# Kernel tuning notes

Hardware: AMD Instinct MI355X
Metric: run time of the kernel (lower is better)

The kernel has to match this reference:

```python
import jax, jax.numpy as jnp
import numpy as np

D = 256      # d_model
NH = 8       # num_heads
NP = 4       # n_points
H = 100      # feature map height (single level)
W = 100      # feature map width
B = 4
Q = H * W
S = H * W


def setup_inputs() -> dict:
    key = jax.random.key(0)
    ks = jax.random.split(key, 12)
    p = lambda k, shp, s=0.02: jax.random.normal(k, shp, jnp.float32) * s
    return {
        "hidden_states": jax.random.normal(ks[0], (B, Q, D), jnp.float32),
        "encoder_hidden_states": jax.random.normal(ks[1], (B, S, D), jnp.float32),
        "reference_points": jax.random.uniform(ks[2], (B, Q, 1, 2), jnp.float32),
        "spatial_shapes": jnp.array([[H, W]], dtype=jnp.int32),
        "W_off": p(ks[3], (NH * NP * 2, D)),
        "b_off": p(ks[4], (NH * NP * 2,), 0.5),
        "W_attn": p(ks[5], (NH * NP, D)),
        "b_attn": jnp.zeros((NH * NP,), jnp.float32),
        "W_val": p(ks[6], (D, D)),
        "b_val": jnp.zeros((D,), jnp.float32),
        "W_out": p(ks[7], (D, D)),
        "b_out": jnp.zeros((D,), jnp.float32),
    }


def _deform_attn(hidden_states, encoder_hidden_states, reference_points,
                 W_off, b_off, W_attn, b_attn, W_val, b_val, W_out, b_out):
    Bsz, Qn, Dm = hidden_states.shape
    d = Dm // NH

    # value projection -> [B, NH, S, d]
    value = (encoder_hidden_states @ W_val.T + b_val).reshape(Bsz, S, NH, d)
    vflat = value.transpose(0, 2, 1, 3).reshape(Bsz * NH, H * W, d)

    # sampling offsets [B,Q,NH,NP,2] (n_levels=1 squeezed)
    off = (hidden_states @ W_off.T + b_off).reshape(Bsz, Qn, NH, NP, 2)
    # attention weights softmax over (n_levels*n_points)=NP -> [B,Q,NH,NP]
    attn = jax.nn.softmax((hidden_states @ W_attn.T + b_attn).reshape(Bsz, Qn, NH, NP), axis=-1)

    # normalized sampling locations: ref + off / [W, H]
    normalizer = jnp.array([W, H], jnp.float32)
    # reference_points: [B,Q,1,2] (level dim) -> broadcast over heads/points
    loc = reference_points[:, :, None, 0, None, :] + off / normalizer  # [B,Q,NH,NP,2]

    # grid_sample semantics: grid = 2*loc - 1, align_corners=False, zeros padding
    gx = 2.0 * loc[..., 0] - 1.0
    gy = 2.0 * loc[..., 1] - 1.0
    x = ((gx + 1.0) * W - 1.0) * 0.5   # pixel coords [B,Q,NH,NP]
    y = ((gy + 1.0) * H - 1.0) * 0.5
    x0 = jnp.floor(x); y0 = jnp.floor(y)
    x1 = x0 + 1.0;     y1 = y0 + 1.0
    wx1 = x - x0; wx0 = 1.0 - wx1
    wy1 = y - y0; wy0 = 1.0 - wy1

    bh = jnp.arange(Bsz * NH)[:, None]

    def corner(xi, yi, wgt):
        valid = (xi >= 0) & (xi <= W - 1) & (yi >= 0) & (yi <= H - 1)
        xi_c = jnp.clip(xi, 0, W - 1).astype(jnp.int32)
        yi_c = jnp.clip(yi, 0, H - 1).astype(jnp.int32)
        idx = (yi_c * W + xi_c).transpose(0, 2, 1, 3).reshape(Bsz * NH, Qn * NP)
        g = vflat[bh, idx]  # [B*NH, Q*NP, d]
        wv = (wgt * valid.astype(wgt.dtype)).transpose(0, 2, 1, 3).reshape(Bsz * NH, Qn * NP, 1)
        return g * wv

    sampled = corner(x0, y0, wx0 * wy0)
    sampled = sampled + corner(x1, y0, wx1 * wy0)
    sampled = sampled + corner(x0, y1, wx0 * wy1)
    sampled = sampled + corner(x1, y1, wx1 * wy1)
    sampled = sampled.reshape(Bsz, NH, Qn, NP, d)

    out = jnp.einsum("bhqpd,bqhp->bqhd", sampled, attn).reshape(Bsz, Qn, Dm)
    return out @ W_out.T + b_out


def reference(hidden_states, encoder_hidden_states, reference_points, spatial_shapes,
              W_off, b_off, W_attn, b_attn, W_val, b_val, W_out, b_out):
    # spatial_shapes is static metadata (must equal [[H, W]]); shapes are baked in.
    return _deform_attn(hidden_states, encoder_hidden_states, reference_points,
                        W_off, b_off, W_attn, b_attn, W_val, b_val, W_out, b_out)
```

## Files before the change

### kernel.cpp

```cpp
#include <hip/hip_runtime.h>

constexpr int HH = 100;
constexpr int WW = 100;
constexpr int NH = 8;
constexpr int NP = 4;
constexpr int B  = 4;
constexpr int Q  = HH * WW;
constexpr int S  = Q;
constexpr int K  = 256;
constexpr int DH = 32;
constexpr int M  = B * Q;
constexpr int NTILES = M / 32;

typedef __attribute__((ext_vector_type(8))) short short8;
typedef __attribute__((ext_vector_type(4))) float f32x4;

__device__ inline unsigned short f2bf(float f) {
    unsigned u = __builtin_bit_cast(unsigned, f);
    u += 0x7fffu + ((u >> 16) & 1u);
    return (unsigned short)(u >> 16);
}
__device__ inline float bf2f(unsigned short h) {
    return __builtin_bit_cast(float, ((unsigned)h) << 16);
}
__device__ inline unsigned short f2h(float f) {
    _Float16 h = (_Float16)f;
    return __builtin_bit_cast(unsigned short, h);
}
__device__ inline float h2f(unsigned short u) {
    return (float)__builtin_bit_cast(_Float16, u);
}

__device__ inline void lds_st16s(short* base, int row, int stride, int kcol, short8 v) {
    *reinterpret_cast<short8*>(&base[row * stride + (kcol ^ ((row & 7) << 3))]) = v;
}
__device__ inline short8 lds_ld16s(const short* base, int row, int stride, int kcol) {
    return *reinterpret_cast<const short8*>(&base[row * stride + (kcol ^ ((row & 7) << 3))]);
}

__device__ inline short8 cvt8(float4 a, float4 b) {
    short8 r;
    r[0] = (short)f2bf(a.x); r[1] = (short)f2bf(a.y);
    r[2] = (short)f2bf(a.z); r[3] = (short)f2bf(a.w);
    r[4] = (short)f2bf(b.x); r[5] = (short)f2bf(b.y);
    r[6] = (short)f2bf(b.z); r[7] = (short)f2bf(b.w);
    return r;
}

__global__ __launch_bounds__(1024) void stage1(
    const float* __restrict__ enc, const float* __restrict__ Wval,
    const float* __restrict__ bval, unsigned short* __restrict__ vflat,
    const float* __restrict__ hidden, const float* __restrict__ Woff,
    const float* __restrict__ Wattn, const float* __restrict__ boff,
    const float* __restrict__ battn, unsigned short* __restrict__ proj)
{
    __shared__ __align__(16) short SM[73728];
    short* Bs = SM;
    short* As = SM + 65536;

    const int tid  = threadIdx.x;
    const int lane = tid & 63, w = tid >> 6;
    const int l15  = lane & 15, l4 = lane >> 4;
    const int arow = tid >> 5, ak = (tid & 31) * 8;

    constexpr int NV = 143, NJ = 113;

    if (blockIdx.x < NV) {
        int t = blockIdx.x;
        float4 fa0, fa1;
        auto lda = [&](int tt) {
            const float* s = &enc[(size_t)(tt * 32 + arow) * K + ak];
            fa0 = *reinterpret_cast<const float4*>(s);
            fa1 = *reinterpret_cast<const float4*>(s + 4);
        };
        lda(t);

        {
            const int brow = tid >> 2, kb = (tid & 3) * 64;
#pragma unroll
            for (int c = 0; c < 8; ++c) {
                const float* s = &Wval[(size_t)brow * 256 + kb + c * 8];
                float4 f0 = *reinterpret_cast<const float4*>(s);
                float4 f1 = *reinterpret_cast<const float4*>(s + 4);
                lds_st16s(Bs, brow, 256, kb + c * 8, cvt8(f0, f1));
            }
        }

        const int n = w * 16 + l15;
        const float bv = bval[n];
        const int h = n >> 5, dd = n & 31;

        for (; t < NTILES; t += NV) {
            lds_st16s(As, arow, 256, ak, cvt8(fa0, fa1));
            __syncthreads();
            if (t + NV < NTILES) lda(t + NV);

            f32x4 acc0 = {0.f, 0.f, 0.f, 0.f}, acc1 = {0.f, 0.f, 0.f, 0.f};
#pragma unroll
            for (int ks = 0; ks < 8; ++ks) {
                const int kc = ks * 32 + l4 * 8;
                const short8 bb = lds_ld16s(Bs, n, 256, kc);
                const short8 a0 = lds_ld16s(As, l15, 256, kc);
                const short8 a1 = lds_ld16s(As, 16 + l15, 256, kc);
                acc0 = __builtin_amdgcn_mfma_f32_16x16x32_bf16(a0, bb, acc0, 0, 0, 0);
                acc1 = __builtin_amdgcn_mfma_f32_16x16x32_bf16(a1, bb, acc1, 0, 0, 0);
            }
            const int m0 = t * 32;
#pragma unroll
            for (int r = 0; r < 4; ++r) {
                int m = m0 + l4 * 4 + r;
                int b_ = m / S, s_ = m - b_ * S;
                vflat[(((size_t)(b_ * NH + h)) * S + s_) * DH + dd] = f2bf(acc0[r] + bv);
                m += 16; b_ = m / S; s_ = m - b_ * S;
                vflat[(((size_t)(b_ * NH + h)) * S + s_) * DH + dd] = f2bf(acc1[r] + bv);
            }
            __syncthreads();
        }
    } else {
        int t = blockIdx.x - NV;
        float4 fa0, fa1;
        auto lda = [&](int tt) {
            const float* s = &hidden[(size_t)(tt * 32 + arow) * K + ak];
            fa0 = *reinterpret_cast<const float4*>(s);
            fa1 = *reinterpret_cast<const float4*>(s + 4);
        };
        lda(t);

        {
#pragma unroll
            for (int j = 0; j < 3; ++j) {
                const int ch = tid * 3 + j;
                const int brow = ch >> 5, kc = (ch & 31) * 8;
                const float* s = (brow < 64)
                    ? &Woff[(size_t)brow * 256 + kc]
                    : &Wattn[(size_t)(brow - 64) * 256 + kc];
                float4 f0 = *reinterpret_cast<const float4*>(s);
                float4 f1 = *reinterpret_cast<const float4*>(s + 4);
                lds_st16s(Bs, brow, 256, kc, cvt8(f0, f1));
            }
        }

        const int nf = w >> 1, mh = w & 1;
        const int n = nf * 16 + l15;
        const float bv = (w < 12) ? ((n < 64) ? boff[n] : battn[n - 64]) : 0.f;

        for (; t < NTILES; t += NJ) {
            lds_st16s(As, arow, 256, ak, cvt8(fa0, fa1));
            __syncthreads();
            if (t + NJ < NTILES) lda(t + NJ);

            if (w < 12) {
                f32x4 acc = {0.f, 0.f, 0.f, 0.f};
#pragma unroll
                for (int ks = 0; ks < 8; ++ks) {
                    const int kc = ks * 32 + l4 * 8;
                    const short8 bb = lds_ld16s(Bs, n, 256, kc);
                    const short8 a = lds_ld16s(As, mh * 16 + l15, 256, kc);
                    acc = __builtin_amdgcn_mfma_f32_16x16x32_bf16(a, bb, acc, 0, 0, 0);
                }
#pragma unroll
                for (int r = 0; r < 4; ++r) {
                    const int m = t * 32 + mh * 16 + l4 * 4 + r;
                    proj[(size_t)m * 96 + n] = f2h(acc[r] + bv);
                }
            }
            __syncthreads();
        }
    }
}

__global__ __launch_bounds__(1024) void sample_out(
    const unsigned short* __restrict__ vflat,
    const unsigned short* __restrict__ proj,
    const float* __restrict__ ref,
    const float* __restrict__ Wout, const float* __restrict__ bout,
    float* __restrict__ out)
{
    __shared__ __align__(16) short SM[73728];
    short* Ws = SM;
    short* Tp = SM + 65536;

    const int tid  = threadIdx.x;
    const int lane = tid & 63, w = tid >> 6;
    const int l15  = lane & 15, l4 = lane >> 4;

    {
        const int brow = tid >> 2, kb = (tid & 3) * 64;
#pragma unroll
        for (int c = 0; c < 8; ++c) {
            const float* s = &Wout[(size_t)brow * 256 + kb + c * 8];
            float4 f0 = *reinterpret_cast<const float4*>(s);
            float4 f1 = *reinterpret_cast<const float4*>(s + 4);
            lds_st16s(Ws, brow, 256, kb + c * 8, cvt8(f0, f1));
        }
    }

    const int n = w * 16 + l15;
    const float bv = bout[n];

    const int r   = tid >> 5;
    const int rem = tid & 31;
    const int h   = rem >> 2;
    const int d0  = (rem & 3) * 8;

    for (int t = blockIdx.x; t < NTILES; t += 256) {
        {
            const int m = t * 32 + r;
            const int b = m / Q;
            const unsigned short* pr = proj + (size_t)m * 96;
            const float refx = ref[(size_t)m * 2 + 0];
            const float refy = ref[(size_t)m * 2 + 1];

            float l[NP];
#pragma unroll
            for (int p = 0; p < NP; ++p) l[p] = h2f(pr[64 + h * 4 + p]);
            const float mx = fmaxf(fmaxf(l[0], l[1]), fmaxf(l[2], l[3]));
            float e[NP]; float esum = 0.f;
#pragma unroll
            for (int p = 0; p < NP; ++p) { e[p] = __expf(l[p] - mx); esum += e[p]; }
            const float inv = 1.f / esum;

            const unsigned short* vbase = vflat + (size_t)(b * NH + h) * (S * DH);

            int   cidx[NP][4];
            float cw[NP][4];
#pragma unroll
            for (int p = 0; p < NP; ++p) {
                const float ox = h2f(pr[h * 8 + p * 2 + 0]);
                const float oy = h2f(pr[h * 8 + p * 2 + 1]);
                const float x = fmaf(refx, (float)WW, ox) - 0.5f;
                const float y = fmaf(refy, (float)HH, oy) - 0.5f;
                const float x0f = floorf(x), y0f = floorf(y);
                const float wx1 = x - x0f, wx0 = 1.f - wx1;
                const float wy1 = y - y0f, wy0 = 1.f - wy1;
                const int x0 = (int)x0f, y0 = (int)y0f;
                const bool vx0 = (x0 >= 0) && (x0 < WW);
                const bool vx1 = (x0 + 1 >= 0) && (x0 + 1 < WW);
                const bool vy0 = (y0 >= 0) && (y0 < HH);
                const bool vy1 = (y0 + 1 >= 0) && (y0 + 1 < HH);
                const int xi0 = min(max(x0, 0), WW - 1);
                const int xi1 = min(max(x0 + 1, 0), WW - 1);
                const int yi0 = min(max(y0, 0), HH - 1);
                const int yi1 = min(max(y0 + 1, 0), HH - 1);
                const float ap = e[p] * inv;
                cw[p][0] = ap * wx0 * wy0 * ((vx0 && vy0) ? 1.f : 0.f);
                cw[p][1] = ap * wx1 * wy0 * ((vx1 && vy0) ? 1.f : 0.f);
                cw[p][2] = ap * wx0 * wy1 * ((vx0 && vy1) ? 1.f : 0.f);
                cw[p][3] = ap * wx1 * wy1 * ((vx1 && vy1) ? 1.f : 0.f);
                cidx[p][0] = (yi0 * WW + xi0) * DH + d0;
                cidx[p][1] = (yi0 * WW + xi1) * DH + d0;
                cidx[p][2] = (yi1 * WW + xi0) * DH + d0;
                cidx[p][3] = (yi1 * WW + xi1) * DH + d0;
            }

            float o[8];
#pragma unroll
            for (int j = 0; j < 8; ++j) o[j] = 0.f;
#pragma unroll
            for (int p = 0; p < NP; ++p) {
#pragma unroll
                for (int c = 0; c < 4; ++c) {
                    const short8 v = *reinterpret_cast<const short8*>(&vbase[cidx[p][c]]);
                    const float wgt = cw[p][c];
#pragma unroll
                    for (int j = 0; j < 8; ++j)
                        o[j] = fmaf(wgt, bf2f((unsigned short)v[j]), o[j]);
                }
            }

            short8 ov;
#pragma unroll
            for (int j = 0; j < 8; ++j) ov[j] = (short)f2bf(o[j]);
            lds_st16s(Tp, r, 256, h * 32 + d0, ov);
        }
        __syncthreads();

        {
            f32x4 acc0 = {0.f, 0.f, 0.f, 0.f}, acc1 = {0.f, 0.f, 0.f, 0.f};
#pragma unroll
            for (int ks = 0; ks < 8; ++ks) {
                const int kc = ks * 32 + l4 * 8;
                const short8 bb = lds_ld16s(Ws, n, 256, kc);
                const short8 a0 = lds_ld16s(Tp, l15, 256, kc);
                const short8 a1 = lds_ld16s(Tp, 16 + l15, 256, kc);
                acc0 = __builtin_amdgcn_mfma_f32_16x16x32_bf16(a0, bb, acc0, 0, 0, 0);
                acc1 = __builtin_amdgcn_mfma_f32_16x16x32_bf16(a1, bb, acc1, 0, 0, 0);
            }
            const int m0 = t * 32;
#pragma unroll
            for (int r2 = 0; r2 < 4; ++r2) {
                const int m = m0 + l4 * 4 + r2;
                out[(size_t)m * K + n] = acc0[r2] + bv;
                out[(size_t)(m + 16) * K + n] = acc1[r2] + bv;
            }
        }
        __syncthreads();
    }
}

extern "C" void kernel_launch(void* const* d_in, const int* in_sizes, int n_in,
                              void* d_out, int out_size, void* d_ws, size_t ws_size,
                              hipStream_t stream)
{
    const float* hidden = (const float*)d_in[0];
    const float* enc    = (const float*)d_in[1];
    const float* refp   = (const float*)d_in[2];
    const float* W_off  = (const float*)d_in[4];
    const float* b_off  = (const float*)d_in[5];
    const float* W_attn = (const float*)d_in[6];
    const float* b_attn = (const float*)d_in[7];
    const float* W_val  = (const float*)d_in[8];
    const float* b_val  = (const float*)d_in[9];
    const float* W_out  = (const float*)d_in[10];
    const float* b_out  = (const float*)d_in[11];
    float* out = (float*)d_out;

    unsigned short* vflat = (unsigned short*)d_ws;
    unsigned short* proj  = vflat + (size_t)10240000;

    stage1<<<256, 1024, 0, stream>>>(
        enc, W_val, b_val, vflat, hidden, W_off, W_attn, b_off, b_attn, proj);

    sample_out<<<256, 1024, 0, stream>>>(vflat, proj, refp, W_out, b_out, out);
}
```

Baseline: 86.04 us.

## Split sampling from out-projection, keep weights in registers, double-buffer A tiles

```diff
diff --git a/kernel.cpp b/kernel.cpp
--- a/kernel.cpp
+++ b/kernel.cpp
@@ -54,9 +54,7 @@
     const float* __restrict__ Wattn, const float* __restrict__ boff,
     const float* __restrict__ battn, unsigned short* __restrict__ proj)
 {
-    __shared__ __align__(16) short SM[73728];
-    short* Bs = SM;
-    short* As = SM + 65536;
+    __shared__ __align__(16) short As[2][32 * 256];
 
     const int tid  = threadIdx.x;
     const int lane = tid & 63, w = tid >> 6;
@@ -66,6 +64,17 @@
     constexpr int NV = 143, NJ = 113;
 
     if (blockIdx.x < NV) {
+        const int n = w * 16 + l15;
+        short8 breg[8];
+#pragma unroll
+        for (int ks = 0; ks < 8; ++ks) {
+            const float* s = &Wval[(size_t)n * K + ks * 32 + l4 * 8];
+            breg[ks] = cvt8(*reinterpret_cast<const float4*>(s),
+                            *reinterpret_cast<const float4*>(s + 4));
+        }
+        const float bv = bval[n];
+        const int h = n >> 5, dd = n & 31;
+
         int t = blockIdx.x;
         float4 fa0, fa1;
         auto lda = [&](int tt) {
@@ -74,36 +83,21 @@
             fa1 = *reinterpret_cast<const float4*>(s + 4);
         };
         lda(t);
-
-        {
-            const int brow = tid >> 2, kb = (tid & 3) * 64;
-#pragma unroll
-            for (int c = 0; c < 8; ++c) {
-                const float* s = &Wval[(size_t)brow * 256 + kb + c * 8];
-                float4 f0 = *reinterpret_cast<const float4*>(s);
-                float4 f1 = *reinterpret_cast<const float4*>(s + 4);
-                lds_st16s(Bs, brow, 256, kb + c * 8, cvt8(f0, f1));
-            }
-        }
-
-        const int n = w * 16 + l15;
-        const float bv = bval[n];
-        const int h = n >> 5, dd = n & 31;
-
+        lds_st16s(As[0], arow, 256, ak, cvt8(fa0, fa1));
+        __syncthreads();
+        int cur = 0;
         for (; t < NTILES; t += NV) {
-            lds_st16s(As, arow, 256, ak, cvt8(fa0, fa1));
-            __syncthreads();
-            if (t + NV < NTILES) lda(t + NV);
+            const bool more = (t + NV < NTILES);
+            if (more) lda(t + NV);
 
             f32x4 acc0 = {0.f, 0.f, 0.f, 0.f}, acc1 = {0.f, 0.f, 0.f, 0.f};
 #pragma unroll
             for (int ks = 0; ks < 8; ++ks) {
                 const int kc = ks * 32 + l4 * 8;
-                const short8 bb = lds_ld16s(Bs, n, 256, kc);
-                const short8 a0 = lds_ld16s(As, l15, 256, kc);
-                const short8 a1 = lds_ld16s(As, 16 + l15, 256, kc);
-                acc0 = __builtin_amdgcn_mfma_f32_16x16x32_bf16(a0, bb, acc0, 0, 0, 0);
-                acc1 = __builtin_amdgcn_mfma_f32_16x16x32_bf16(a1, bb, acc1, 0, 0, 0);
+                const short8 a0 = lds_ld16s(As[cur], l15, 256, kc);
+                const short8 a1 = lds_ld16s(As[cur], 16 + l15, 256, kc);
+                acc0 = __builtin_amdgcn_mfma_f32_16x16x32_bf16(a0, breg[ks], acc0, 0, 0, 0);
+                acc1 = __builtin_amdgcn_mfma_f32_16x16x32_bf16(a1, breg[ks], acc1, 0, 0, 0);
             }
             const int m0 = t * 32;
 #pragma unroll
@@ -114,9 +108,27 @@
                 m += 16; b_ = m / S; s_ = m - b_ * S;
                 vflat[(((size_t)(b_ * NH + h)) * S + s_) * DH + dd] = f2bf(acc1[r] + bv);
             }
+            if (more) lds_st16s(As[cur ^ 1], arow, 256, ak, cvt8(fa0, fa1));
             __syncthreads();
+            cur ^= 1;
         }
     } else {
+        const int nf = w >> 1, mh = w & 1;
+        const int n = nf * 16 + l15;
+        short8 breg[8];
+        float bv = 0.f;
+        if (w < 12) {
+#pragma unroll
+            for (int ks = 0; ks < 8; ++ks) {
+                const float* s = (n < 64)
+                    ? &Woff[(size_t)n * K + ks * 32 + l4 * 8]
+                    : &Wattn[(size_t)(n - 64) * K + ks * 32 + l4 * 8];
+                breg[ks] = cvt8(*reinterpret_cast<const float4*>(s),
+                                *reinterpret_cast<const float4*>(s + 4));
+            }
+            bv = (n < 64) ? boff[n] : battn[n - 64];
+        }
+
         int t = blockIdx.x - NV;
         float4 fa0, fa1;
         auto lda = [&](int tt) {
@@ -125,38 +137,20 @@
             fa1 = *reinterpret_cast<const float4*>(s + 4);
         };
         lda(t);
-
-        {
-#pragma unroll
-            for (int j = 0; j < 3; ++j) {
-                const int ch = tid * 3 + j;
-                const int brow = ch >> 5, kc = (ch & 31) * 8;
-                const float* s = (brow < 64)
-                    ? &Woff[(size_t)brow * 256 + kc]
-                    : &Wattn[(size_t)(brow - 64) * 256 + kc];
-                float4 f0 = *reinterpret_cast<const float4*>(s);
-                float4 f1 = *reinterpret_cast<const float4*>(s + 4);
-                lds_st16s(Bs, brow, 256, kc, cvt8(f0, f1));
-            }
-        }
-
-        const int nf = w >> 1, mh = w & 1;
-        const int n = nf * 16 + l15;
-        const float bv = (w < 12) ? ((n < 64) ? boff[n] : battn[n - 64]) : 0.f;
-
+        lds_st16s(As[0], arow, 256, ak, cvt8(fa0, fa1));
+        __syncthreads();
+        int cur = 0;
         for (; t < NTILES; t += NJ) {
-            lds_st16s(As, arow, 256, ak, cvt8(fa0, fa1));
-            __syncthreads();
-            if (t + NJ < NTILES) lda(t + NJ);
+            const bool more = (t + NJ < NTILES);
+            if (more) lda(t + NJ);
 
             if (w < 12) {
                 f32x4 acc = {0.f, 0.f, 0.f, 0.f};
 #pragma unroll
                 for (int ks = 0; ks < 8; ++ks) {
                     const int kc = ks * 32 + l4 * 8;
-                    const short8 bb = lds_ld16s(Bs, n, 256, kc);
-                    const short8 a = lds_ld16s(As, mh * 16 + l15, 256, kc);
-                    acc = __builtin_amdgcn_mfma_f32_16x16x32_bf16(a, bb, acc, 0, 0, 0);
+                    const short8 a = lds_ld16s(As[cur], mh * 16 + l15, 256, kc);
+                    acc = __builtin_amdgcn_mfma_f32_16x16x32_bf16(a, breg[ks], acc, 0, 0, 0);
                 }
 #pragma unroll
                 for (int r = 0; r < 4; ++r) {
@@ -164,137 +158,155 @@
                     proj[(size_t)m * 96 + n] = f2h(acc[r] + bv);
                 }
             }
+            if (more) lds_st16s(As[cur ^ 1], arow, 256, ak, cvt8(fa0, fa1));
             __syncthreads();
-        }
-    }
-}
-
-__global__ __launch_bounds__(1024) void sample_out(
+            cur ^= 1;
+        }
+    }
+}
+
+__global__ __launch_bounds__(256) void sample_agg(
     const unsigned short* __restrict__ vflat,
     const unsigned short* __restrict__ proj,
     const float* __restrict__ ref,
-    const float* __restrict__ Wout, const float* __restrict__ bout,
-    float* __restrict__ out)
+    unsigned short* __restrict__ tmp)
 {
-    __shared__ __align__(16) short SM[73728];
-    short* Ws = SM;
-    short* Tp = SM + 65536;
+    const int nblk = gridDim.x;
+    const int cpx  = nblk >> 3;
+    const int swz  = (blockIdx.x & 7) * cpx + (blockIdx.x >> 3);
+
+    const int lg   = threadIdx.x >> 2;
+    const int lane = threadIdx.x & 3;
+    const int d0   = lane * 8;
+
+    const int g  = swz * 64 + lg;
+    const int q  = g % Q;
+    const int bh = g / Q;
+    const int b  = bh >> 3;
+    const int h  = bh & 7;
+
+    const size_t bq = (size_t)b * Q + q;
+    const float refx = ref[bq * 2 + 0];
+    const float refy = ref[bq * 2 + 1];
+    const unsigned short* pr = proj + bq * 96;
+
+    float l[NP];
+#pragma unroll
+    for (int p = 0; p < NP; ++p) l[p] = h2f(pr[64 + h * 4 + p]);
+    const float mx = fmaxf(fmaxf(l[0], l[1]), fmaxf(l[2], l[3]));
+    float e[NP];
+    float esum = 0.f;
+#pragma unroll
+    for (int p = 0; p < NP; ++p) { e[p] = __expf(l[p] - mx); esum += e[p]; }
+    const float inv = 1.f / esum;
+
+    const unsigned short* vbase = vflat + (size_t)bh * (S * DH);
+
+    int   cidx[NP][4];
+    float cw[NP][4];
+#pragma unroll
+    for (int p = 0; p < NP; ++p) {
+        const float ox = h2f(pr[h * 8 + p * 2 + 0]);
+        const float oy = h2f(pr[h * 8 + p * 2 + 1]);
+        const float x = fmaf(refx, (float)WW, ox) - 0.5f;
+        const float y = fmaf(refy, (float)HH, oy) - 0.5f;
+        const float x0f = floorf(x), y0f = floorf(y);
+        const float wx1 = x - x0f, wx0 = 1.f - wx1;
+        const float wy1 = y - y0f, wy0 = 1.f - wy1;
+        const int x0 = (int)x0f, y0 = (int)y0f;
+        const bool vx0 = (x0 >= 0) && (x0 < WW);
+        const bool vx1 = (x0 + 1 >= 0) && (x0 + 1 < WW);
+        const bool vy0 = (y0 >= 0) && (y0 < HH);
+        const bool vy1 = (y0 + 1 >= 0) && (y0 + 1 < HH);
+        const int xi0 = min(max(x0, 0), WW - 1);
+        const int xi1 = min(max(x0 + 1, 0), WW - 1);
+        const int yi0 = min(max(y0, 0), HH - 1);
+        const int yi1 = min(max(y0 + 1, 0), HH - 1);
+        const float ap = e[p] * inv;
+        cw[p][0] = ap * wx0 * wy0 * ((vx0 && vy0) ? 1.f : 0.f);
+        cw[p][1] = ap * wx1 * wy0 * ((vx1 && vy0) ? 1.f : 0.f);
+        cw[p][2] = ap * wx0 * wy1 * ((vx0 && vy1) ? 1.f : 0.f);
+        cw[p][3] = ap * wx1 * wy1 * ((vx1 && vy1) ? 1.f : 0.f);
+        cidx[p][0] = (yi0 * WW + xi0) * DH + d0;
+        cidx[p][1] = (yi0 * WW + xi1) * DH + d0;
+        cidx[p][2] = (yi1 * WW + xi0) * DH + d0;
+        cidx[p][3] = (yi1 * WW + xi1) * DH + d0;
+    }
+
+    float o[8];
+#pragma unroll
+    for (int j = 0; j < 8; ++j) o[j] = 0.f;
+#pragma unroll
+    for (int p = 0; p < NP; ++p) {
+#pragma unroll
+        for (int c = 0; c < 4; ++c) {
+            const short8 v = *reinterpret_cast<const short8*>(&vbase[cidx[p][c]]);
+            const float wgt = cw[p][c];
+#pragma unroll
+            for (int j = 0; j < 8; ++j)
+                o[j] = fmaf(wgt, bf2f((unsigned short)v[j]), o[j]);
+        }
+    }
+
+    short8 ov;
+#pragma unroll
+    for (int j = 0; j < 8; ++j) ov[j] = (short)f2bf(o[j]);
+    *reinterpret_cast<short8*>(&tmp[bq * 256 + h * 32 + d0]) = ov;
+}
+
+__global__ __launch_bounds__(1024) void out_proj(
+    const unsigned short* __restrict__ tmp, const float* __restrict__ Wo,
+    const float* __restrict__ bo, float* __restrict__ out)
+{
+    __shared__ __align__(16) short As[2][32 * 256];
 
     const int tid  = threadIdx.x;
     const int lane = tid & 63, w = tid >> 6;
     const int l15  = lane & 15, l4 = lane >> 4;
-
-    {
-        const int brow = tid >> 2, kb = (tid & 3) * 64;
-#pragma unroll
-        for (int c = 0; c < 8; ++c) {
-            const float* s = &Wout[(size_t)brow * 256 + kb + c * 8];
-            float4 f0 = *reinterpret_cast<const float4*>(s);
-            float4 f1 = *reinterpret_cast<const float4*>(s + 4);
-            lds_st16s(Ws, brow, 256, kb + c * 8, cvt8(f0, f1));
-        }
-    }
+    const int arow = tid >> 5, ak = (tid & 31) * 8;
 
     const int n = w * 16 + l15;
-    const float bv = bout[n];
-
-    const int r   = tid >> 5;
-    const int rem = tid & 31;
-    const int h   = rem >> 2;
-    const int d0  = (rem & 3) * 8;
-
-    for (int t = blockIdx.x; t < NTILES; t += 256) {
-        {
-            const int m = t * 32 + r;
-            const int b = m / Q;
-            const unsigned short* pr = proj + (size_t)m * 96;
-            const float refx = ref[(size_t)m * 2 + 0];
-            const float refy = ref[(size_t)m * 2 + 1];
-
-            float l[NP];
-#pragma unroll
-            for (int p = 0; p < NP; ++p) l[p] = h2f(pr[64 + h * 4 + p]);
-            const float mx = fmaxf(fmaxf(l[0], l[1]), fmaxf(l[2], l[3]));
-            float e[NP]; float esum = 0.f;
-#pragma unroll
-            for (int p = 0; p < NP; ++p) { e[p] = __expf(l[p] - mx); esum += e[p]; }
-            const float inv = 1.f / esum;
-
-            const unsigned short* vbase = vflat + (size_t)(b * NH + h) * (S * DH);
-
-            int   cidx[NP][4];
-            float cw[NP][4];
-#pragma unroll
-            for (int p = 0; p < NP; ++p) {
-                const float ox = h2f(pr[h * 8 + p * 2 + 0]);
-                const float oy = h2f(pr[h * 8 + p * 2 + 1]);
-                const float x = fmaf(refx, (float)WW, ox) - 0.5f;
-                const float y = fmaf(refy, (float)HH, oy) - 0.5f;
-                const float x0f = floorf(x), y0f = floorf(y);
-                const float wx1 = x - x0f, wx0 = 1.f - wx1;
-                const float wy1 = y - y0f, wy0 = 1.f - wy1;
-                const int x0 = (int)x0f, y0 = (int)y0f;
-                const bool vx0 = (x0 >= 0) && (x0 < WW);
-                const bool vx1 = (x0 + 1 >= 0) && (x0 + 1 < WW);
-                const bool vy0 = (y0 >= 0) && (y0 < HH);
-                const bool vy1 = (y0 + 1 >= 0) && (y0 + 1 < HH);
-                const int xi0 = min(max(x0, 0), WW - 1);
-                const int xi1 = min(max(x0 + 1, 0), WW - 1);
-                const int yi0 = min(max(y0, 0), HH - 1);
-                const int yi1 = min(max(y0 + 1, 0), HH - 1);
-                const float ap = e[p] * inv;
-                cw[p][0] = ap * wx0 * wy0 * ((vx0 && vy0) ? 1.f : 0.f);
-                cw[p][1] = ap * wx1 * wy0 * ((vx1 && vy0) ? 1.f : 0.f);
-                cw[p][2] = ap * wx0 * wy1 * ((vx0 && vy1) ? 1.f : 0.f);
-                cw[p][3] = ap * wx1 * wy1 * ((vx1 && vy1) ? 1.f : 0.f);
-                cidx[p][0] = (yi0 * WW + xi0) * DH + d0;
-                cidx[p][1] = (yi0 * WW + xi1) * DH + d0;
-                cidx[p][2] = (yi1 * WW + xi0) * DH + d0;
-                cidx[p][3] = (yi1 * WW + xi1) * DH + d0;
-            }
-
-            float o[8];
-#pragma unroll
-            for (int j = 0; j < 8; ++j) o[j] = 0.f;
-#pragma unroll
-            for (int p = 0; p < NP; ++p) {
-#pragma unroll
-                for (int c = 0; c < 4; ++c) {
-                    const short8 v = *reinterpret_cast<const short8*>(&vbase[cidx[p][c]]);
-                    const float wgt = cw[p][c];
-#pragma unroll
-                    for (int j = 0; j < 8; ++j)
-                        o[j] = fmaf(wgt, bf2f((unsigned short)v[j]), o[j]);
-                }
-            }
-
-            short8 ov;
-#pragma unroll
-            for (int j = 0; j < 8; ++j) ov[j] = (short)f2bf(o[j]);
-            lds_st16s(Tp, r, 256, h * 32 + d0, ov);
-        }
+    short8 breg[8];
+#pragma unroll
+    for (int ks = 0; ks < 8; ++ks) {
+        const float* s = &Wo[(size_t)n * K + ks * 32 + l4 * 8];
+        breg[ks] = cvt8(*reinterpret_cast<const float4*>(s),
+                        *reinterpret_cast<const float4*>(s + 4));
+    }
+    const float bv = bo[n];
+
+    int t = blockIdx.x;
+    short8 sa;
+    auto lda = [&](int tt) {
+        sa = *reinterpret_cast<const short8*>(&tmp[(size_t)(tt * 32 + arow) * K + ak]);
+    };
+    lda(t);
+    lds_st16s(As[0], arow, 256, ak, sa);
+    __syncthreads();
+    int cur = 0;
+    for (; t < NTILES; t += 256) {
+        const bool more = (t + 256 < NTILES);
+        if (more) lda(t + 256);
+
+        f32x4 acc0 = {0.f, 0.f, 0.f, 0.f}, acc1 = {0.f, 0.f, 0.f, 0.f};
+#pragma unroll
+        for (int ks = 0; ks < 8; ++ks) {
+            const int kc = ks * 32 + l4 * 8;
+            const short8 a0 = lds_ld16s(As[cur], l15, 256, kc);
+            const short8 a1 = lds_ld16s(As[cur], 16 + l15, 256, kc);
+            acc0 = __builtin_amdgcn_mfma_f32_16x16x32_bf16(a0, breg[ks], acc0, 0, 0, 0);
+            acc1 = __builtin_amdgcn_mfma_f32_16x16x32_bf16(a1, breg[ks], acc1, 0, 0, 0);
+        }
+        const int m0 = t * 32;
+#pragma unroll
+        for (int r = 0; r < 4; ++r) {
+            const int m = m0 + l4 * 4 + r;
+            out[(size_t)m * K + n] = acc0[r] + bv;
+            out[(size_t)(m + 16) * K + n] = acc1[r] + bv;
+        }
+        if (more) lds_st16s(As[cur ^ 1], arow, 256, ak, sa);
         __syncthreads();
-
-        {
-            f32x4 acc0 = {0.f, 0.f, 0.f, 0.f}, acc1 = {0.f, 0.f, 0.f, 0.f};
-#pragma unroll
-            for (int ks = 0; ks < 8; ++ks) {
-                const int kc = ks * 32 + l4 * 8;
-                const short8 bb = lds_ld16s(Ws, n, 256, kc);
-                const short8 a0 = lds_ld16s(Tp, l15, 256, kc);
-                const short8 a1 = lds_ld16s(Tp, 16 + l15, 256, kc);
-                acc0 = __builtin_amdgcn_mfma_f32_16x16x32_bf16(a0, bb, acc0, 0, 0, 0);
-                acc1 = __builtin_amdgcn_mfma_f32_16x16x32_bf16(a1, bb, acc1, 0, 0, 0);
-            }
-            const int m0 = t * 32;
-#pragma unroll
-            for (int r2 = 0; r2 < 4; ++r2) {
-                const int m = m0 + l4 * 4 + r2;
-                out[(size_t)m * K + n] = acc0[r2] + bv;
-                out[(size_t)(m + 16) * K + n] = acc1[r2] + bv;
-            }
-        }
-        __syncthreads();
+        cur ^= 1;
     }
 }
 
@@ -317,9 +329,12 @@
 
     unsigned short* vflat = (unsigned short*)d_ws;
     unsigned short* proj  = vflat + (size_t)10240000;
+    unsigned short* tmp   = proj + (size_t)3840000;
 
     stage1<<<256, 1024, 0, stream>>>(
         enc, W_val, b_val, vflat, hidden, W_off, W_attn, b_off, b_attn, proj);
 
-    sample_out<<<256, 1024, 0, stream>>>(vflat, proj, refp, W_out, b_out, out);
-}
+    sample_agg<<<5000, 256, 0, stream>>>(vflat, proj, refp, tmp);
+
+    out_proj<<<256, 1024, 0, stream>>>(tmp, W_out, b_out, out);
+}
```

Result: faster. 72.97 us (-15.2%).
